# Performance work log

Hardware: AMD Instinct MI355X
Metric: run time of the kernel (lower is better)

## Reference

```python
import jax, jax.numpy as jnp
import numpy as np
import math

L = 12      # n_layer (alternating adaptive True/False)
H = 8       # n_head
C = 256     # n_embd
DH = C // H # head dim = 32
BS = 828    # block_size
T = 827     # seq len after dropping last token
VOCAB = 16384
CAM = 30
IMG = 256


def get_sinusoid(n_position, d_hid):
    pos = np.arange(n_position)[:, None].astype(np.float64)
    hid = np.arange(d_hid)[None, :]
    angle = pos / np.power(10000.0, 2.0 * (hid // 2) / d_hid)
    table = np.zeros_like(angle)
    table[:, 0::2] = np.sin(angle[:, 0::2])
    table[:, 1::2] = np.cos(angle[:, 1::2])
    return jnp.asarray(table[None], jnp.float32)  # [1, n_position, d_hid]


def layer_norm(x, w, b):
    m = x.mean(-1, keepdims=True)
    v = ((x - m) ** 2).mean(-1, keepdims=True)
    return (x - m) * jax.lax.rsqrt(v + 1e-5) * w + b


def setup_inputs() -> dict:
    key = jax.random.key(0)
    ks = iter(jax.random.split(key, 64))
    nrm = lambda shape, s=1.0: jax.random.normal(next(ks), shape, jnp.float32) * s
    B = 4
    inp = {
        'dc_emb': nrm((B, 572, C)),
        'z_emb': nrm((B, 256, C)),
        'p1': nrm((B, CAM)),
        'p2': nrm((B, CAM)),
        'p3': nrm((B, CAM)),
        'frame_emb': nrm((1, 256, C), 0.02),
        'camera_emb': nrm((1, 30, C), 0.02),
        'time_emb': get_sinusoid(BS, C),
        'loc_W1': nrm((2 * CAM, CAM), 0.02), 'loc_b1': jnp.zeros((2 * CAM,)),
        'loc_W2': nrm((IMG * IMG, 2 * CAM), 0.02), 'loc_b2': jnp.zeros((IMG * IMG,)),
        'ln1_w': jnp.ones((L, C)), 'ln1_b': jnp.zeros((L, C)),
        'Wq': nrm((L, C, C), 0.02), 'bq': jnp.zeros((L, C)),
        'Wk': nrm((L, C, C), 0.02), 'bk': jnp.zeros((L, C)),
        'Wv': nrm((L, C, C), 0.02), 'bv': jnp.zeros((L, C)),
        'Wo': nrm((L, C, C), 0.02), 'bo': jnp.zeros((L, C)),
        'ln2_w': jnp.ones((L, C)), 'ln2_b': jnp.zeros((L, C)),
        'W1': nrm((L, 4 * C, C), 0.02), 'b1': jnp.zeros((L, 4 * C)),
        'W2': nrm((L, C, 4 * C), 0.02), 'b2': jnp.zeros((L, C)),
        'lnf_w': jnp.ones((C,)), 'lnf_b': jnp.zeros((C,)),
        'head_W': nrm((VOCAB, C), 0.02),
    }
    return inp


def _forward(dc_emb, z_emb, p1, p2, p3, frame_emb, camera_emb, time_emb,
             loc_W1, loc_b1, loc_W2, loc_b2,
             ln1_w, ln1_b, Wq, bq, Wk, bk, Wv, bv, Wo, bo,
             ln2_w, ln2_b, W1, b1, W2, b2, lnf_w, lnf_b, head_W):
    B = dc_emb.shape[0]
    scale = 1.0 / math.sqrt(DH)

    # AdaptiveAttention bias h: [B, 1, BS, BS] with three 256x256 learned blocks
    def locality(p):
        z = jax.nn.gelu(p @ loc_W1.T + loc_b1, approximate=False)
        z = z @ loc_W2.T + loc_b2
        return z.reshape(B, IMG, IMG)

    h = jnp.zeros((B, 1, BS, BS), dc_emb.dtype)
    h = h.at[:, 0, 285:541, 0:256].set(locality(p1))
    h = h.at[:, 0, 571:827, 0:256].set(locality(p2))
    h = h.at[:, 0, 571:827, 286:542].set(locality(p3))
    h = h[:, :, :T, :T]

    # token + role + time embeddings
    tok = jnp.concatenate([dc_emb, z_emb], axis=1)[:, :-1, :]  # [B, T, C]
    role = jnp.concatenate([frame_emb, camera_emb, frame_emb, camera_emb, frame_emb], axis=1)[:, :T, :]
    x = tok + role + time_emb[:, :T, :]

    causal = jnp.tril(jnp.ones((T, T), bool))  # [T, T]

    for i in range(L):
        adaptive = (i % 2 == 0)
        xn = layer_norm(x, ln1_w[i], ln1_b[i])
        q = (xn @ Wq[i].T + bq[i]).reshape(B, T, H, DH)
        k = (xn @ Wk[i].T + bk[i]).reshape(B, T, H, DH)
        v = (xn @ Wv[i].T + bv[i]).reshape(B, T, H, DH)
        att = jnp.einsum('bqhd,bkhd->bhqk', q, k) * scale
        if adaptive:
            att = att + h
        att = jnp.where(causal, att, -jnp.inf)
        att = jax.nn.softmax(att, axis=-1)
        y = jnp.einsum('bhqk,bkhd->bqhd', att, v).reshape(B, T, C)
        x = x + y @ Wo[i].T + bo[i]
        xn2 = layer_norm(x, ln2_w[i], ln2_b[i])
        x = x + jax.nn.gelu(xn2 @ W1[i].T + b1[i], approximate=False) @ W2[i].T + b2[i]

    x = layer_norm(x, lnf_w, lnf_b)
    logits = x @ head_W.T  # [B, T, VOCAB]
    return logits


def reference(dc_emb, z_emb, p1, p2, p3, frame_emb, camera_emb, time_emb,
              loc_W1, loc_b1, loc_W2, loc_b2,
              ln1_w, ln1_b, Wq, bq, Wk, bk, Wv, bv, Wo, bo,
              ln2_w, ln2_b, W1, b1, W2, b2, lnf_w, lnf_b, head_W):
    return _forward(dc_emb, z_emb, p1, p2, p3, frame_emb, camera_emb, time_emb,
                    loc_W1, loc_b1, loc_W2, loc_b2,
                    ln1_w, ln1_b, Wq, bq, Wk, bk, Wv, bv, Wo, bo,
                    ln2_w, ln2_b, W1, b1, W2, b2, lnf_w, lnf_b, head_W)
```

## Files before the change

kernel.cpp:

```cpp
#include <hip/hip_runtime.h>
#include <hip/hip_bf16.h>
#include <math.h>

#define T_LEN 827
#define M_ROWS 3308
#define NLAYER 12
#define NEG_SENT -1e30f

typedef __attribute__((ext_vector_type(4))) float f32x4;
typedef __attribute__((ext_vector_type(8))) short bf16x8;

__device__ __forceinline__ float gelu_f(float x) {
    return 0.5f * x * (1.0f + erff(x * 0.70710678118654752440f));
}

__device__ __forceinline__ short f2bf_s(float x) {
    __hip_bfloat16 h = __float2bfloat16(x);
    return *reinterpret_cast<short*>(&h);
}

__global__ void cvt_kernel(const float* __restrict__ in, __hip_bfloat16* __restrict__ out, int n4) {
    int i = blockIdx.x * blockDim.x + threadIdx.x;
    if (i >= n4) return;
    float4 v = reinterpret_cast<const float4*>(in)[i];
    out[4*i+0] = __float2bfloat16(v.x);
    out[4*i+1] = __float2bfloat16(v.y);
    out[4*i+2] = __float2bfloat16(v.z);
    out[4*i+3] = __float2bfloat16(v.w);
}

__global__ void prep_wqkv_kernel(const float* __restrict__ Wq, const float* __restrict__ Wk,
                                 const float* __restrict__ Wv, __hip_bfloat16* __restrict__ out) {
    int i = blockIdx.x * 256 + threadIdx.x;
    if (i >= 12*768*64) return;
    int el = i * 4;
    int layer = el / (768*256);
    int rem = el % (768*256);
    int row = rem >> 8, col = rem & 255;
    const float* src;
    float sc = 1.f;
    if (row < 256)      { src = Wq + ((size_t)layer*256 + row)*256 + col; sc = 0.17677669529663687f; }
    else if (row < 512) { src = Wk + ((size_t)layer*256 + (row-256))*256 + col; }
    else                { src = Wv + ((size_t)layer*256 + (row-512))*256 + col; }
    float4 v = *reinterpret_cast<const float4*>(src);
    out[el+0] = __float2bfloat16(v.x * sc);
    out[el+1] = __float2bfloat16(v.y * sc);
    out[el+2] = __float2bfloat16(v.z * sc);
    out[el+3] = __float2bfloat16(v.w * sc);
}

__global__ void prep_bqkv_kernel(const float* __restrict__ bq, const float* __restrict__ bk,
                                 const float* __restrict__ bv, float* __restrict__ out) {
    int i = blockIdx.x * 256 + threadIdx.x;
    if (i >= 12*768) return;
    int layer = i / 768, row = i % 768;
    float v;
    if (row < 256)      v = bq[layer*256 + row] * 0.17677669529663687f;
    else if (row < 512) v = bk[layer*256 + (row-256)];
    else                v = bv[layer*256 + (row-512)];
    out[i] = v;
// ... 103 lines not shown
            *reinterpret_cast<uint4*>(&Bs[r][sg*8 + j*32]) =
                *reinterpret_cast<const uint4*>(bsrc + j*32);
    }
    int gr = m0 + r; if (gr > M-1) gr = M-1;
    {
        const __hip_bfloat16* asrc = Abf + (size_t)gr * 256 + sg * 8;
        #pragma unroll
        for (int j = 0; j < 8; ++j)
            *reinterpret_cast<uint4*>(&As[r][sg*8 + j*32]) =
                *reinterpret_cast<const uint4*>(asrc + j*32);
    }
    __syncthreads();

    const int wid = tid >> 6, lane = tid & 63;
    const int wm = wid >> 1, wn = wid & 1, c = lane & 15, g = lane >> 4;
    f32x4 acc[2][2];
    #pragma unroll
    for (int mi = 0; mi < 2; ++mi)
        #pragma unroll
        for (int ni = 0; ni < 2; ++ni)
            acc[mi][ni] = (f32x4){0.f, 0.f, 0.f, 0.f};

    #pragma unroll
    for (int kj = 0; kj < 8; ++kj) {
        bf16x8 a0 = *reinterpret_cast<const bf16x8*>(&As[wm*32 + c][kj*32 + g*8]);
        bf16x8 a1 = *reinterpret_cast<const bf16x8*>(&As[wm*32 + 16 + c][kj*32 + g*8]);
        bf16x8 b0 = *reinterpret_cast<const bf16x8*>(&Bs[wn*32 + c][kj*32 + g*8]);
        bf16x8 b1v = *reinterpret_cast<const bf16x8*>(&Bs[wn*32 + 16 + c][kj*32 + g*8]);
        acc[0][0] = __builtin_amdgcn_mfma_f32_16x16x32_bf16(a0, b0, acc[0][0], 0, 0, 0);
        acc[0][1] = __builtin_amdgcn_mfma_f32_16x16x32_bf16(a0, b1v, acc[0][1], 0, 0, 0);
        acc[1][0] = __builtin_amdgcn_mfma_f32_16x16x32_bf16(a1, b0, acc[1][0], 0, 0, 0);
        acc[1][1] = __builtin_amdgcn_mfma_f32_16x16x32_bf16(a1, b1v, acc[1][1], 0, 0, 0);
    }

    #pragma unroll
    for (int mi = 0; mi < 2; ++mi) {
        #pragma unroll
        for (int ni = 0; ni < 2; ++ni) {
            int n = n0 + wn*32 + ni*16 + c;
            float bb = bias ? bias[n] : 0.f;
            #pragma unroll
            for (int rg = 0; rg < 4; ++rg) {
                int m = m0 + wm*32 + mi*16 + g*4 + rg;
                if (m >= M) continue;
                float v = acc[mi][ni][rg] + bb;
                if (RESID) v += resid[(size_t)m*N + n];
                if (OUTBF16) ((__hip_bfloat16*)out)[(size_t)m*N + n] = __float2bfloat16(v);
                else         ((float*)out)[(size_t)m*N + n] = v;
            }
        }
    }
}

__global__ __launch_bounds__(512) void mlp_fused(
    float* __restrict__ x,
    const float* __restrict__ ln2w, const float* __restrict__ ln2b,
    const __hip_bfloat16* __restrict__ W1, const float* __restrict__ b1,
    const __hip_bfloat16* __restrict__ W2, const float* __restrict__ b2,
    const float* __restrict__ lnow, const float* __restrict__ lnob,
    __hip_bfloat16* __restrict__ xn)
{
    __shared__ __hip_bfloat16 As[32][264];
    __shared__ __hip_bfloat16 Ms[32][1044];
    const int tid = threadIdx.x;
    const int m0 = blockIdx.x * 32;
    const int w = tid >> 6, lane = tid & 63, c = lane & 15, g = lane >> 4;

    {
        int r = tid >> 4, p = tid & 15;
        int gr = m0 + r; if (gr > M_ROWS-1) gr = M_ROWS-1;
        const float* src = x + (size_t)gr*256 + p*16;
        float4 f0 = *reinterpret_cast<const float4*>(src);
        float4 f1 = *reinterpret_cast<const float4*>(src + 4);
        float4 f2 = *reinterpret_cast<const float4*>(src + 8);
        float4 f3 = *reinterpret_cast<const float4*>(src + 12);
        float vv[16] = {f0.x,f0.y,f0.z,f0.w, f1.x,f1.y,f1.z,f1.w,
                        f2.x,f2.y,f2.z,f2.w, f3.x,f3.y,f3.z,f3.w};
        float s = 0.f, q = 0.f;
        #pragma unroll
        for (int e = 0; e < 16; ++e) { s += vv[e]; q += vv[e]*vv[e]; }
        #pragma unroll
        for (int msk = 1; msk <= 8; msk <<= 1) { s += __shfl_xor(s, msk); q += __shfl_xor(q, msk); }
        float mean = s * (1.f/256.f);
        float rstd = rsqrtf(q*(1.f/256.f) - mean*mean + 1e-5f);
        bf16x8 pk0, pk1;
        #pragma unroll
        for (int e = 0; e < 8; ++e) {
            pk0[e] = f2bf_s((vv[e]   - mean)*rstd*ln2w[p*16+e]   + ln2b[p*16+e]);
            pk1[e] = f2bf_s((vv[8+e] - mean)*rstd*ln2w[p*16+8+e] + ln2b[p*16+8+e]);
        }
        *reinterpret_cast<bf16x8*>(&As[r][p*16])     = pk0;
        *reinterpret_cast<bf16x8*>(&As[r][p*16 + 8]) = pk1;
    }
    __syncthreads();

    #pragma unroll 1
    for (int ns = 0; ns < 8; ++ns) {
        int nb = w*128 + ns*16;
        const __hip_bfloat16* wrow = W1 + (size_t)(nb + c)*256 + g*8;
        f32x4 a0 = (f32x4){0.f,0.f,0.f,0.f}, a1 = (f32x4){0.f,0.f,0.f,0.f};
        #pragma unroll
        for (int kj = 0; kj < 8; ++kj) {
            bf16x8 bfrag = *reinterpret_cast<const bf16x8*>(wrow + kj*32);
            bf16x8 af0 = *reinterpret_cast<const bf16x8*>(&As[c][kj*32 + g*8]);
            bf16x8 af1 = *reinterpret_cast<const bf16x8*>(&As[16 + c][kj*32 + g*8]);
            a0 = __builtin_amdgcn_mfma_f32_16x16x32_bf16(af0, bfrag, a0, 0, 0, 0);
            a1 = __builtin_amdgcn_mfma_f32_16x16x32_bf16(af1, bfrag, a1, 0, 0, 0);
        }
        float bb = b1[nb + c];
        #pragma unroll
        for (int rg = 0; rg < 4; ++rg) {
            Ms[g*4 + rg][nb + c]      = __float2bfloat16(gelu_f(a0[rg] + bb));
            Ms[16 + g*4 + rg][nb + c] = __float2bfloat16(gelu_f(a1[rg] + bb));
        }
    }
    __syncthreads();

    f32x4 o[2][2];
    #pragma unroll
    for (int i = 0; i < 2; ++i)
        #pragma unroll
        for (int j = 0; j < 2; ++j)
            o[i][j] = (f32x4){0.f,0.f,0.f,0.f};
    #pragma unroll
    for (int ns2 = 0; ns2 < 2; ++ns2) {
        int nb = w*32 + ns2*16;
        const __hip_bfloat16* wrow = W2 + (size_t)(nb + c)*1024 + g*8;
        #pragma unroll
        for (int kj = 0; kj < 32; ++kj) {
            bf16x8 bfrag = *reinterpret_cast<const bf16x8*>(wrow + kj*32);
            bf16x8 af0 = *reinterpret_cast<const bf16x8*>(&Ms[c][kj*32 + g*8]);
            bf16x8 af1 = *reinterpret_cast<const bf16x8*>(&Ms[16 + c][kj*32 + g*8]);
            o[ns2][0] = __builtin_amdgcn_mfma_f32_16x16x32_bf16(af0, bfrag, o[ns2][0], 0, 0, 0);
            o[ns2][1] = __builtin_amdgcn_mfma_f32_16x16x32_bf16(af1, bfrag, o[ns2][1], 0, 0, 0);
        }
    }
    __syncthreads();

    float* xf = reinterpret_cast<float*>(&Ms[0][0]);
    #pragma unroll
    for (int ns2 = 0; ns2 < 2; ++ns2) {
        int nb = w*32 + ns2*16;
        float bb = b2[nb + c];
        #pragma unroll
        for (int mi = 0; mi < 2; ++mi) {
            #pragma unroll
            for (int rg = 0; rg < 4; ++rg) {
                int row = mi*16 + g*4 + rg;
                int gm = m0 + row;
                if (gm < M_ROWS) {
                    float v = o[ns2][mi][rg] + bb + x[(size_t)gm*256 + nb + c];
                    x[(size_t)gm*256 + nb + c] = v;
                    xf[row*256 + nb + c] = v;
                }
            }
        }
    }
    __syncthreads();

    {
        int r = tid >> 4, p = tid & 15;
        int gm = m0 + r;
        const float* src = xf + r*256 + p*16;
        float4 f0 = *reinterpret_cast<const float4*>(src);
        float4 f1 = *reinterpret_cast<const float4*>(src + 4);
        float4 f2 = *reinterpret_cast<const float4*>(src + 8);
        float4 f3 = *reinterpret_cast<const float4*>(src + 12);
        float vv[16] = {f0.x,f0.y,f0.z,f0.w, f1.x,f1.y,f1.z,f1.w,
                        f2.x,f2.y,f2.z,f2.w, f3.x,f3.y,f3.z,f3.w};
        float s = 0.f, q = 0.f;
        #pragma unroll
        for (int e = 0; e < 16; ++e) { s += vv[e]; q += vv[e]*vv[e]; }
        #pragma unroll
        for (int msk = 1; msk <= 8; msk <<= 1) { s += __shfl_xor(s, msk); q += __shfl_xor(q, msk); }
        float mean = s * (1.f/256.f);
        float rstd = rsqrtf(q*(1.f/256.f) - mean*mean + 1e-5f);
        if (gm < M_ROWS) {
            bf16x8 pk0, pk1;
            #pragma unroll
            for (int e = 0; e < 8; ++e) {
                pk0[e] = f2bf_s((vv[e]   - mean)*rstd*lnow[p*16+e]   + lnob[p*16+e]);
                pk1[e] = f2bf_s((vv[8+e] - mean)*rstd*lnow[p*16+8+e] + lnob[p*16+8+e]);
            }
            *reinterpret_cast<bf16x8*>(&xn[(size_t)gm*256 + p*16])     = pk0;
            *reinterpret_cast<bf16x8*>(&xn[(size_t)gm*256 + p*16 + 8]) = pk1;
        }
    }
}

template<int ADAPT>
__global__ __launch_bounds__(512) void attn_v3_kernel(const __hip_bfloat16* __restrict__ qkv,
                                                      const __hip_bfloat16* __restrict__ hbuf,
                                                      __hip_bfloat16* __restrict__ y) {
    const int qi = blockIdx.x, hh = blockIdx.y, b = blockIdx.z;
    const int tid = threadIdx.x;
    const int w = tid >> 6, lane = tid & 63;
    const int c = lane & 15, g = lane >> 4;
    const int qsub = w & 3, grp = w >> 2;
    const int q0 = qi * 64;
    const int qw0 = q0 + qsub * 16;
    const int nt = qi + 1;
    const int h = (nt + 1) >> 1;

    __shared__ short Ks[2][2][64][40];
    __shared__ short Vt[2][2][32][68];
    __shared__ short Pw[8][16][72];
    __shared__ float mlS[4][16][2];

    int qrow = qw0 + c; if (qrow > T_LEN-1) qrow = T_LEN-1;
    bf16x8 aq = *reinterpret_cast<const bf16x8*>(qkv + ((size_t)b*T_LEN + qrow)*768 + hh*32 + g*8);

    float m_r[4] = {NEG_SENT, NEG_SENT, NEG_SENT, NEG_SENT};
    float l_r[4] = {0.f, 0.f, 0.f, 0.f};
    f32x4 acc[2];
    acc[0] = (f32x4){0.f,0.f,0.f,0.f};
    acc[1] = (f32x4){0.f,0.f,0.f,0.f};

    const int lt = tid & 255;
    const int srow = lt >> 2;
    const int scol8 = (lt & 3) * 8;

    bf16x8 kreg, vreg;
    {
        int kb0 = (grp ? h : 0) * 64;
        int krow = kb0 + srow; if (krow > T_LEN-1) krow = T_LEN-1;
        const __hip_bfloat16* gb = qkv + ((size_t)b*T_LEN + krow)*768 + hh*32 + scol8;
        kreg = *reinterpret_cast<const bf16x8*>(gb + 256);
        vreg = *reinterpret_cast<const bf16x8*>(gb + 512);
    }

    for (int it = 0; it < h; ++it) {
        const int bsel = it & 1;
        const int kb = (grp ? h + it : it) * 64;
        *reinterpret_cast<bf16x8*>(&Ks[grp][bsel][srow][scol8]) = kreg;
        #pragma unroll
        for (int jj = 0; jj < 8; ++jj) Vt[grp][bsel][scol8 + jj][srow] = vreg[jj];
        __syncthreads();
        if (it + 1 < h) {
            int kbn = (grp ? h + it + 1 : it + 1) * 64;
            int krow = kbn + srow; if (krow > T_LEN-1) krow = T_LEN-1;
            const __hip_bfloat16* gb = qkv + ((size_t)b*T_LEN + krow)*768 + hh*32 + scol8;
            kreg = *reinterpret_cast<const bf16x8*>(gb + 256);
            vreg = *reinterpret_cast<const bf16x8*>(gb + 512);
        }

        f32x4 sc4[4];
        #pragma unroll
        for (int j = 0; j < 4; ++j) {
            bf16x8 bk = *reinterpret_cast<const bf16x8*>(&Ks[grp][bsel][j*16 + c][g*8]);
            sc4[j] = __builtin_amdgcn_mfma_f32_16x16x32_bf16(aq, bk, (f32x4){0.f,0.f,0.f,0.f}, 0, 0, 0);
        }

        float sv[4][4];
        #pragma unroll
        for (int j = 0; j < 4; ++j) {
            int kk = kb + j*16 + c;
            #pragma unroll
            for (int rg = 0; rg < 4; ++rg) {
                int qq = qw0 + g*4 + rg;
                bool valid = (qq < T_LEN) && (kk <= qq);
                float s = sc4[j][rg];
                if (ADAPT) s += valid ? __bfloat162float(hbuf[((size_t)b*T_LEN + qq)*T_LEN + kk]) : 0.f;
                sv[j][rg] = valid ? s : NEG_SENT;
            }
        }

        float sf[4];
        #pragma unroll
        for (int rg = 0; rg < 4; ++rg) {
            float m = fmaxf(fmaxf(sv[0][rg], sv[1][rg]), fmaxf(sv[2][rg], sv[3][rg]));
            #pragma unroll
            for (int msk = 1; msk <= 8; msk <<= 1) m = fmaxf(m, __shfl_xor(m, msk));
            float mn = fmaxf(m_r[rg], m);
            sf[rg] = __expf(m_r[rg] - mn);
            m_r[rg] = mn;
        }
        float p[4][4];
        #pragma unroll
        for (int rg = 0; rg < 4; ++rg) {
            float su = 0.f;
            #pragma unroll
            for (int j = 0; j < 4; ++j) {
                float e = __expf(sv[j][rg] - m_r[rg]);
                p[j][rg] = e;
                su += e;
            }
            #pragma unroll
            for (int msk = 1; msk <= 8; msk <<= 1) su += __shfl_xor(su, msk);
            l_r[rg] = l_r[rg] * sf[rg] + su;
            acc[0][rg] *= sf[rg];
            acc[1][rg] *= sf[rg];
        }

        #pragma unroll
        for (int j = 0; j < 4; ++j)
            #pragma unroll
            for (int rg = 0; rg < 4; ++rg)
                Pw[w][g*4 + rg][j*16 + c] = f2bf_s(p[j][rg]);

        #pragma unroll
        for (int kc = 0; kc < 2; ++kc) {
            bf16x8 ap = *reinterpret_cast<const bf16x8*>(&Pw[w][c][kc*32 + g*8]);
            #pragma unroll
            for (int dt = 0; dt < 2; ++dt) {
                bf16x8 bv = *reinterpret_cast<const bf16x8*>(&Vt[grp][bsel][dt*16 + c][kc*32 + g*8]);
                acc[dt] = __builtin_amdgcn_mfma_f32_16x16x32_bf16(ap, bv, acc[dt], 0, 0, 0);
            }
        }
    }

    if (grp == 1) {
        float* accS = reinterpret_cast<float*>(&Pw[4 + qsub][0][0]);
        #pragma unroll
        for (int rg = 0; rg < 4; ++rg) {
            int row = g*4 + rg;
            accS[row*32 + c]      = acc[0][rg];
            accS[row*32 + 16 + c] = acc[1][rg];
            if (c == 0) { mlS[qsub][row][0] = m_r[rg]; mlS[qsub][row][1] = l_r[rg]; }
        }
    }
    __syncthreads();
    if (grp == 0) {
        const float* accS = reinterpret_cast<const float*>(&Pw[4 + qsub][0][0]);
        #pragma unroll
        for (int rg = 0; rg < 4; ++rg) {
            int row = g*4 + rg;
            int qq = qw0 + row;
            if (qq >= T_LEN) continue;
            float m1 = mlS[qsub][row][0], l1 = mlS[qsub][row][1];
            float M = fmaxf(m_r[rg], m1);
            float a = __expf(m_r[rg] - M);
            float bsc = __expf(m1 - M);
            float L = l_r[rg]*a + l1*bsc;
            float inv = 1.f / L;
            float o0 = (acc[0][rg]*a + accS[row*32 + c]*bsc) * inv;
            float o1 = (acc[1][rg]*a + accS[row*32 + 16 + c]*bsc) * inv;
            size_t yo = ((size_t)b*T_LEN + qq)*256 + hh*32;
            y[yo + c]      = __float2bfloat16(o0);
            y[yo + 16 + c] = __float2bfloat16(o1);
        }
    }
}

extern "C" void kernel_launch(void* const* d_in, const int* in_sizes, int n_in,
                              void* d_out, int out_size, void* d_ws, size_t ws_size,
                              hipStream_t stream) {
    const float* dc    = (const float*)d_in[0];
    const float* zemb  = (const float*)d_in[1];
    const float* p1    = (const float*)d_in[2];
    const float* p2    = (const float*)d_in[3];
    const float* p3    = (const float*)d_in[4];
    const float* frame = (const float*)d_in[5];
    const float* cam   = (const float*)d_in[6];
    const float* timeE = (const float*)d_in[7];
    const float* locW1 = (const float*)d_in[8];
    const float* locb1 = (const float*)d_in[9];
    const float* locW2 = (const float*)d_in[10];
    const float* locb2 = (const float*)d_in[11];
    const float* ln1w  = (const float*)d_in[12];
    const float* ln1b  = (const float*)d_in[13];
    const float* Wq    = (const float*)d_in[14];
    const float* bq    = (const float*)d_in[15];
    const float* Wk    = (const float*)d_in[16];
    const float* bk    = (const float*)d_in[17];
    const float* Wv    = (const float*)d_in[18];
    const float* bv    = (const float*)d_in[19];
    const float* Wo    = (const float*)d_in[20];
    const float* bo    = (const float*)d_in[21];
    const float* ln2w  = (const float*)d_in[22];
    const float* ln2b  = (const float*)d_in[23];
    const float* W1p   = (const float*)d_in[24];
    const float* b1p   = (const float*)d_in[25];
    const float* W2p   = (const float*)d_in[26];
    const float* b2p   = (const float*)d_in[27];
    const float* lnfw  = (const float*)d_in[28];
    const float* lnfb  = (const float*)d_in[29];
    const float* headW = (const float*)d_in[30];

    char* wsb = (char*)d_ws;
    size_t off = 0;
    auto alloc = [&](size_t bytes) -> char* {
        char* p = wsb + off;
        off += (bytes + 255) & ~(size_t)255;
        return p;
    };
    __hip_bfloat16* wqkv_bf = (__hip_bfloat16*)alloc(12ull*768*256*2);
    float*          bqkv    = (float*)alloc(12ull*768*4);
    __hip_bfloat16* wo_bf = (__hip_bfloat16*)alloc(12ull*65536*2);
    __hip_bfloat16* w1_bf = (__hip_bfloat16*)alloc(12ull*262144*2);
    __hip_bfloat16* w2_bf = (__hip_bfloat16*)alloc(12ull*262144*2);
    __hip_bfloat16* wh_bf = (__hip_bfloat16*)alloc(16384ull*256*2);
    __hip_bfloat16* hbuf = (__hip_bfloat16*)alloc(4ull*T_LEN*T_LEN*2);
    float* x    = (float*)alloc((size_t)M_ROWS*256*4);
    __hip_bfloat16* xn   = (__hip_bfloat16*)alloc((size_t)M_ROWS*256*2);
    __hip_bfloat16* qkvb = (__hip_bfloat16*)alloc((size_t)M_ROWS*768*2);
    __hip_bfloat16* yb   = (__hip_bfloat16*)alloc((size_t)M_ROWS*256*2);
    float* z1   = (float*)alloc(720*4);

    prep_wqkv_kernel<<<(12*768*64 + 255)/256, 256, 0, stream>>>(Wq, Wk, Wv, wqkv_bf);
    prep_bqkv_kernel<<<36, 256, 0, stream>>>(bq, bk, bv, bqkv);
    cvt_kernel<<<768, 256, 0, stream>>>(Wo, wo_bf, 196608);
    cvt_kernel<<<3072, 256, 0, stream>>>(W1p, w1_bf, 786432);
    cvt_kernel<<<3072, 256, 0, stream>>>(W2p, w2_bf, 786432);
    cvt_kernel<<<4096, 256, 0, stream>>>(headW, wh_bf, 1048576);

    loc_z1_kernel<<<1, 256, 0, stream>>>(p1, p2, p3, locW1, locb1, z1);
    zero_kernel<<<2048, 256, 0, stream>>>((float*)hbuf, (4*T_LEN*T_LEN)/2);
    h_fill_kernel<<<256, 256, 0, stream>>>(z1, locW2, locb2, hbuf);

    init_x_kernel<<<M_ROWS, 256, 0, stream>>>(dc, zemb, frame, cam, timeE, x);
    ln_kernel<<<M_ROWS, 256, 0, stream>>>(x, ln1w, ln1b, xn);

    dim3 gqkv(52, 12);
    dim3 goproj(52, 4);
    dim3 gattn(13, 8, 4);

    for (int i = 0; i < NLAYER; ++i) {
        gemm_k256<false,true><<<gqkv, 256, 0, stream>>>(
            xn, wqkv_bf + (size_t)i*196608, bqkv + i*768, nullptr, qkvb, M_ROWS, 768);
        if (i % 2 == 0) attn_v3_kernel<1><<<gattn, 512, 0, stream>>>(qkvb, hbuf, yb);
        else            attn_v3_kernel<0><<<gattn, 512, 0, stream>>>(qkvb, hbuf, yb);
        gemm_k256<true,false><<<goproj, 256, 0, stream>>>(
            yb, wo_bf + (size_t)i*65536, bo + i*256, x, x, M_ROWS, 256);
        const float* lnow = (i == NLAYER-1) ? lnfw : (ln1w + (i+1)*256);
        const float* lnob = (i == NLAYER-1) ? lnfb : (ln1b + (i+1)*256);
        mlp_fused<<<104, 512, 0, stream>>>(
            x, ln2w + i*256, ln2b + i*256,
            w1_bf + (size_t)i*262144, b1p + i*1024,
            w2_bf + (size_t)i*262144, b2p + i*256, lnow, lnob, xn);
    }

    gemm_k256<false,false><<<dim3(52, 256), 256, 0, stream>>>(
        xn, wh_bf, nullptr, nullptr, (float*)d_out, M_ROWS, 16384);
}
```

Before: 1.249 ms.

## Emit transposed V from QKV GEMM and stream K/V from global in attention

The QKV projection becomes a dedicated kernel that writes Q/K into a 512-wide buffer and V pre-transposed per batch and head into a padded buffer. Attention now gives each wavefront its own 16-query tile, reading K and V^T straight from global memory into registers with register prefetch. This removes LDS staging, block-wide barriers and the split-KV merge step. In exchange each wave reloads K/V from global or L2 with no sharing across waves, the block shrinks to 256 threads, and the V writes in the GEMM epilogue are scattered.

```diff
diff --git a/kernel.cpp b/kernel.cpp
--- a/kernel.cpp
+++ b/kernel.cpp
@@ -6,6 +6,7 @@
 #define M_ROWS 3308
 #define NLAYER 12
 #define NEG_SENT -1e30f
+#define VT_W 896
 
 typedef __attribute__((ext_vector_type(4))) float f32x4;
 typedef __attribute__((ext_vector_type(8))) short bf16x8;
@@ -215,6 +216,83 @@
     }
 }
 
+__global__ __launch_bounds__(256) void gemm_qkv256(
+    const __hip_bfloat16* __restrict__ Abf,
+    const __hip_bfloat16* __restrict__ W, const float* __restrict__ bias,
+    __hip_bfloat16* __restrict__ qkout, __hip_bfloat16* __restrict__ vTout)
+{
+    __shared__ __hip_bfloat16 As[64][264];
+    __shared__ __hip_bfloat16 Bs[64][264];
+    const int tid = threadIdx.x;
+    const int m0 = blockIdx.x * 64, n0 = blockIdx.y * 64;
+    const int r = tid >> 2, sg = tid & 3;
+
+    {
+        const __hip_bfloat16* bsrc = W + (size_t)(n0 + r) * 256 + sg * 8;
+        #pragma unroll
+        for (int j = 0; j < 8; ++j)
+            *reinterpret_cast<uint4*>(&Bs[r][sg*8 + j*32]) =
+                *reinterpret_cast<const uint4*>(bsrc + j*32);
+    }
+    int gr = m0 + r; if (gr > M_ROWS-1) gr = M_ROWS-1;
+    {
+        const __hip_bfloat16* asrc = Abf + (size_t)gr * 256 + sg * 8;
+        #pragma unroll
+        for (int j = 0; j < 8; ++j)
+            *reinterpret_cast<uint4*>(&As[r][sg*8 + j*32]) =
+                *reinterpret_cast<const uint4*>(asrc + j*32);
+    }
+    __syncthreads();
+
+    const int wid = tid >> 6, lane = tid & 63;
+    const int wm = wid >> 1, wn = wid & 1, c = lane & 15, g = lane >> 4;
+    f32x4 acc[2][2];
+    #pragma unroll
+    for (int mi = 0; mi < 2; ++mi)
+        #pragma unroll
+        for (int ni = 0; ni < 2; ++ni)
+            acc[mi][ni] = (f32x4){0.f, 0.f, 0.f, 0.f};
+
+    #pragma unroll
+    for (int kj = 0; kj < 8; ++kj) {
+        bf16x8 a0 = *reinterpret_cast<const bf16x8*>(&As[wm*32 + c][kj*32 + g*8]);
+        bf16x8 a1 = *reinterpret_cast<const bf16x8*>(&As[wm*32 + 16 + c][kj*32 + g*8]);
+        bf16x8 b0 = *reinterpret_cast<const bf16x8*>(&Bs[wn*32 + c][kj*32 + g*8]);
+        bf16x8 b1v = *reinterpret_cast<const bf16x8*>(&Bs[wn*32 + 16 + c][kj*32 + g*8]);
+        acc[0][0] = __builtin_amdgcn_mfma_f32_16x16x32_bf16(a0, b0, acc[0][0], 0, 0, 0);
+        acc[0][1] = __builtin_amdgcn_mfma_f32_16x16x32_bf16(a0, b1v, acc[0][1], 0, 0, 0);
+        acc[1][0] = __builtin_amdgcn_mfma_f32_16x16x32_bf16(a1, b0, acc[1][0], 0, 0, 0);
+        acc[1][1] = __builtin_amdgcn_mfma_f32_16x16x32_bf16(a1, b1v, acc[1][1], 0, 0, 0);
+    }
+
+    #pragma unroll
+    for (int mi = 0; mi < 2; ++mi) {
+        #pragma unroll
+        for (int ni = 0; ni < 2; ++ni) {
+            int n = n0 + wn*32 + ni*16 + c;
+            float bb = bias[n];
+            if (n < 512) {
+                #pragma unroll
+                for (int rg = 0; rg < 4; ++rg) {
+                    int m = m0 + wm*32 + mi*16 + g*4 + rg;
+                    if (m >= M_ROWS) continue;
+                    qkout[(size_t)m*512 + n] = __float2bfloat16(acc[mi][ni][rg] + bb);
+                }
+            } else {
+                int rel = n - 512, hh = rel >> 5, dh = rel & 31;
+                #pragma unroll
+                for (int rg = 0; rg < 4; ++rg) {
+                    int m = m0 + wm*32 + mi*16 + g*4 + rg;
+                    if (m >= M_ROWS) continue;
+                    int bq = m / T_LEN, t = m - bq*T_LEN;
+                    vTout[((size_t)((bq*8 + hh)*32) + dh)*VT_W + t] =
+                        __float2bfloat16(acc[mi][ni][rg] + bb);
+                }
+            }
+        }
+    }
+}
+
 __global__ __launch_bounds__(512) void mlp_fused(
     float* __restrict__ x,
     const float* __restrict__ ln2w, const float* __restrict__ ln2b,
@@ -352,26 +430,26 @@
 }
 
 template<int ADAPT>
-__global__ __launch_bounds__(512) void attn_v3_kernel(const __hip_bfloat16* __restrict__ qkv,
+__global__ __launch_bounds__(256) void attn_v4_kernel(const __hip_bfloat16* __restrict__ qk,
+                                                      const __hip_bfloat16* __restrict__ vT,
                                                       const __hip_bfloat16* __restrict__ hbuf,
                                                       __hip_bfloat16* __restrict__ y) {
-    const int qi = blockIdx.x, hh = blockIdx.y, b = blockIdx.z;
+    const int hh = blockIdx.y, b = blockIdx.z;
     const int tid = threadIdx.x;
     const int w = tid >> 6, lane = tid & 63;
     const int c = lane & 15, g = lane >> 4;
-    const int qsub = w & 3, grp = w >> 2;
-    const int q0 = qi * 64;
-    const int qw0 = q0 + qsub * 16;
-    const int nt = qi + 1;
-    const int h = (nt + 1) >> 1;
-
-    __shared__ short Ks[2][2][64][40];
-    __shared__ short Vt[2][2][32][68];
-    __shared__ short Pw[8][16][72];
-    __shared__ float mlS[4][16][2];
-
-    int qrow = qw0 + c; if (qrow > T_LEN-1) qrow = T_LEN-1;
-    bf16x8 aq = *reinterpret_cast<const bf16x8*>(qkv + ((size_t)b*T_LEN + qrow)*768 + hh*32 + g*8);
+    const int jt = blockIdx.x * 4 + w;
+    const int q0 = jt * 16;
+    const int nit = (q0 + 15) / 64 + 1;
+
+    __shared__ short Pw[4][16][72];
+
+    const size_t qkb = (size_t)b * T_LEN * 512;
+    int qrow = q0 + c; if (qrow > T_LEN-1) qrow = T_LEN-1;
+    bf16x8 aq = *reinterpret_cast<const bf16x8*>(qk + qkb + (size_t)qrow*512 + hh*32 + g*8);
+
+    const __hip_bfloat16* kbase = qk + qkb + 256 + hh*32 + g*8;
+    const __hip_bfloat16* vbase = vT + (size_t)((b*8 + hh)*32)*VT_W + g*8;
 
     float m_r[4] = {NEG_SENT, NEG_SENT, NEG_SENT, NEG_SENT};
     float l_r[4] = {0.f, 0.f, 0.f, 0.f};
@@ -379,52 +457,52 @@
     acc[0] = (f32x4){0.f,0.f,0.f,0.f};
     acc[1] = (f32x4){0.f,0.f,0.f,0.f};
 
-    const int lt = tid & 255;
-    const int srow = lt >> 2;
-    const int scol8 = (lt & 3) * 8;
-
-    bf16x8 kreg, vreg;
-    {
-        int kb0 = (grp ? h : 0) * 64;
-        int krow = kb0 + srow; if (krow > T_LEN-1) krow = T_LEN-1;
-        const __hip_bfloat16* gb = qkv + ((size_t)b*T_LEN + krow)*768 + hh*32 + scol8;
-        kreg = *reinterpret_cast<const bf16x8*>(gb + 256);
-        vreg = *reinterpret_cast<const bf16x8*>(gb + 512);
-    }
-
-    for (int it = 0; it < h; ++it) {
-        const int bsel = it & 1;
-        const int kb = (grp ? h + it : it) * 64;
-        *reinterpret_cast<bf16x8*>(&Ks[grp][bsel][srow][scol8]) = kreg;
-        #pragma unroll
-        for (int jj = 0; jj < 8; ++jj) Vt[grp][bsel][scol8 + jj][srow] = vreg[jj];
-        __syncthreads();
-        if (it + 1 < h) {
-            int kbn = (grp ? h + it + 1 : it + 1) * 64;
-            int krow = kbn + srow; if (krow > T_LEN-1) krow = T_LEN-1;
-            const __hip_bfloat16* gb = qkv + ((size_t)b*T_LEN + krow)*768 + hh*32 + scol8;
-            kreg = *reinterpret_cast<const bf16x8*>(gb + 256);
-            vreg = *reinterpret_cast<const bf16x8*>(gb + 512);
-        }
+    bf16x8 bk[4], bv[2][2];
+    #pragma unroll
+    for (int jj = 0; jj < 4; ++jj) {
+        int krow = jj*16 + c; if (krow > T_LEN-1) krow = T_LEN-1;
+        bk[jj] = *reinterpret_cast<const bf16x8*>(kbase + (size_t)krow*512);
+    }
+    #pragma unroll
+    for (int dt = 0; dt < 2; ++dt)
+        #pragma unroll
+        for (int kc = 0; kc < 2; ++kc)
+            bv[dt][kc] = *reinterpret_cast<const bf16x8*>(vbase + (size_t)(dt*16 + c)*VT_W + kc*32);
+
+    for (int it = 0; it < nit; ++it) {
+        const int kb = it * 64;
 
         f32x4 sc4[4];
         #pragma unroll
-        for (int j = 0; j < 4; ++j) {
-            bf16x8 bk = *reinterpret_cast<const bf16x8*>(&Ks[grp][bsel][j*16 + c][g*8]);
-            sc4[j] = __builtin_amdgcn_mfma_f32_16x16x32_bf16(aq, bk, (f32x4){0.f,0.f,0.f,0.f}, 0, 0, 0);
+        for (int jj = 0; jj < 4; ++jj)
+            sc4[jj] = __builtin_amdgcn_mfma_f32_16x16x32_bf16(aq, bk[jj], (f32x4){0.f,0.f,0.f,0.f}, 0, 0, 0);
+
+        bf16x8 nk[4], nv[2][2];
+        if (it + 1 < nit) {
+            const int kbn = kb + 64;
+            #pragma unroll
+            for (int jj = 0; jj < 4; ++jj) {
+                int krow = kbn + jj*16 + c; if (krow > T_LEN-1) krow = T_LEN-1;
+                nk[jj] = *reinterpret_cast<const bf16x8*>(kbase + (size_t)krow*512);
+            }
+            #pragma unroll
+            for (int dt = 0; dt < 2; ++dt)
+                #pragma unroll
+                for (int kc = 0; kc < 2; ++kc)
+                    nv[dt][kc] = *reinterpret_cast<const bf16x8*>(vbase + (size_t)(dt*16 + c)*VT_W + kbn + kc*32);
         }
 
         float sv[4][4];
         #pragma unroll
-        for (int j = 0; j < 4; ++j) {
-            int kk = kb + j*16 + c;
+        for (int jj = 0; jj < 4; ++jj) {
+            int kk = kb + jj*16 + c;
             #pragma unroll
             for (int rg = 0; rg < 4; ++rg) {
-                int qq = qw0 + g*4 + rg;
+                int qq = q0 + g*4 + rg;
                 bool valid = (qq < T_LEN) && (kk <= qq);
-                float s = sc4[j][rg];
+                float s = sc4[jj][rg];
                 if (ADAPT) s += valid ? __bfloat162float(hbuf[((size_t)b*T_LEN + qq)*T_LEN + kk]) : 0.f;
-                sv[j][rg] = valid ? s : NEG_SENT;
+                sv[jj][rg] = valid ? s : NEG_SENT;
             }
         }
 
@@ -443,9 +521,9 @@
         for (int rg = 0; rg < 4; ++rg) {
             float su = 0.f;
             #pragma unroll
-            for (int j = 0; j < 4; ++j) {
-                float e = __expf(sv[j][rg] - m_r[rg]);
-                p[j][rg] = e;
+            for (int jj = 0; jj < 4; ++jj) {
+                float e = __expf(sv[jj][rg] - m_r[rg]);
+                p[jj][rg] = e;
                 su += e;
             }
             #pragma unroll
@@ -456,52 +534,37 @@
         }
 
         #pragma unroll
-        for (int j = 0; j < 4; ++j)
+        for (int jj = 0; jj < 4; ++jj)
             #pragma unroll
             for (int rg = 0; rg < 4; ++rg)
-                Pw[w][g*4 + rg][j*16 + c] = f2bf_s(p[j][rg]);
+                Pw[w][g*4 + rg][jj*16 + c] = f2bf_s(p[jj][rg]);
 
         #pragma unroll
         for (int kc = 0; kc < 2; ++kc) {
             bf16x8 ap = *reinterpret_cast<const bf16x8*>(&Pw[w][c][kc*32 + g*8]);
             #pragma unroll
-            for (int dt = 0; dt < 2; ++dt) {
-                bf16x8 bv = *reinterpret_cast<const bf16x8*>(&Vt[grp][bsel][dt*16 + c][kc*32 + g*8]);
-                acc[dt] = __builtin_amdgcn_mfma_f32_16x16x32_bf16(ap, bv, acc[dt], 0, 0, 0);
-            }
-        }
-    }
-
-    if (grp == 1) {
-        float* accS = reinterpret_cast<float*>(&Pw[4 + qsub][0][0]);
-        #pragma unroll
-        for (int rg = 0; rg < 4; ++rg) {
-            int row = g*4 + rg;
-            accS[row*32 + c]      = acc[0][rg];
-            accS[row*32 + 16 + c] = acc[1][rg];
-            if (c == 0) { mlS[qsub][row][0] = m_r[rg]; mlS[qsub][row][1] = l_r[rg]; }
-        }
-    }
-    __syncthreads();
-    if (grp == 0) {
-        const float* accS = reinterpret_cast<const float*>(&Pw[4 + qsub][0][0]);
-        #pragma unroll
-        for (int rg = 0; rg < 4; ++rg) {
-            int row = g*4 + rg;
-            int qq = qw0 + row;
-            if (qq >= T_LEN) continue;
-            float m1 = mlS[qsub][row][0], l1 = mlS[qsub][row][1];
-            float M = fmaxf(m_r[rg], m1);
-            float a = __expf(m_r[rg] - M);
-            float bsc = __expf(m1 - M);
-            float L = l_r[rg]*a + l1*bsc;
-            float inv = 1.f / L;
-            float o0 = (acc[0][rg]*a + accS[row*32 + c]*bsc) * inv;
-            float o1 = (acc[1][rg]*a + accS[row*32 + 16 + c]*bsc) * inv;
-            size_t yo = ((size_t)b*T_LEN + qq)*256 + hh*32;
-            y[yo + c]      = __float2bfloat16(o0);
-            y[yo + 16 + c] = __float2bfloat16(o1);
-        }
+            for (int dt = 0; dt < 2; ++dt)
+                acc[dt] = __builtin_amdgcn_mfma_f32_16x16x32_bf16(ap, bv[dt][kc], acc[dt], 0, 0, 0);
+        }
+
+        if (it + 1 < nit) {
+            #pragma unroll
+            for (int jj = 0; jj < 4; ++jj) bk[jj] = nk[jj];
+            #pragma unroll
+            for (int dt = 0; dt < 2; ++dt)
+                #pragma unroll
+                for (int kc = 0; kc < 2; ++kc) bv[dt][kc] = nv[dt][kc];
+        }
+    }
+
+    #pragma unroll
+    for (int rg = 0; rg < 4; ++rg) {
+        int qq = q0 + g*4 + rg;
+        if (qq >= T_LEN) continue;
+        float inv = 1.f / l_r[rg];
+        size_t yo = ((size_t)b*T_LEN + qq)*256 + hh*32;
+        y[yo + c]      = __float2bfloat16(acc[0][rg] * inv);
+        y[yo + 16 + c] = __float2bfloat16(acc[1][rg] * inv);
     }
 }
 
@@ -556,7 +619,8 @@
     __hip_bfloat16* hbuf = (__hip_bfloat16*)alloc(4ull*T_LEN*T_LEN*2);
     float* x    = (float*)alloc((size_t)M_ROWS*256*4);
     __hip_bfloat16* xn   = (__hip_bfloat16*)alloc((size_t)M_ROWS*256*2);
-    __hip_bfloat16* qkvb = (__hip_bfloat16*)alloc((size_t)M_ROWS*768*2);
+    __hip_bfloat16* qkb  = (__hip_bfloat16*)alloc((size_t)M_ROWS*512*2);
+    __hip_bfloat16* vTb  = (__hip_bfloat16*)alloc(1024ull*VT_W*2);
     __hip_bfloat16* yb   = (__hip_bfloat16*)alloc((size_t)M_ROWS*256*2);
     float* z1   = (float*)alloc(720*4);
 
@@ -579,10 +643,10 @@
     dim3 gattn(13, 8, 4);
 
     for (int i = 0; i < NLAYER; ++i) {
-        gemm_k256<false,true><<<gqkv, 256, 0, stream>>>(
-            xn, wqkv_bf + (size_t)i*196608, bqkv + i*768, nullptr, qkvb, M_ROWS, 768);
-        if (i % 2 == 0) attn_v3_kernel<1><<<gattn, 512, 0, stream>>>(qkvb, hbuf, yb);
-        else            attn_v3_kernel<0><<<gattn, 512, 0, stream>>>(qkvb, hbuf, yb);
+        gemm_qkv256<<<gqkv, 256, 0, stream>>>(
+            xn, wqkv_bf + (size_t)i*196608, bqkv + i*768, qkb, vTb);
+        if (i % 2 == 0) attn_v4_kernel<1><<<gattn, 256, 0, stream>>>(qkb, vTb, hbuf, yb);
+        else            attn_v4_kernel<0><<<gattn, 256, 0, stream>>>(qkb, vTb, hbuf, yb);
         gemm_k256<true,false><<<goproj, 256, 0, stream>>>(
             yb, wo_bf + (size_t)i*65536, bo + i*256, x, x, M_ROWS, 256);
         const float* lnow = (i == NLAYER-1) ? lnfw : (ln1w + (i+1)*256);
```

New measurement: 1.483 ms. 1.19x slower.

## Halve MLP row tile and replace split-K attention with single-group 128-key tiles

Applied to the files above, without the earlier changes.

The fused MLP kernel now processes 16 rows per block instead of 32, doubling the grid to 207 blocks so more CUs are busy, at the cost of reading each weight matrix twice as often. The attention kernel drops its two-group key split with cross-group softmax merge and register double buffering. It now uses 256 threads, each block walking key tiles of 128 with a single flash-style online softmax. This removes the merge step and the shared-memory reduction, but loses load prefetch overlap and serialises the key loop per block.

```diff
diff --git a/kernel.cpp b/kernel.cpp
--- a/kernel.cpp
+++ b/kernel.cpp
@@ -223,37 +223,31 @@
     const float* __restrict__ lnow, const float* __restrict__ lnob,
     __hip_bfloat16* __restrict__ xn)
 {
-    __shared__ __hip_bfloat16 As[32][264];
-    __shared__ __hip_bfloat16 Ms[32][1044];
+    __shared__ __hip_bfloat16 As[16][264];
+    __shared__ __hip_bfloat16 Ms[16][1044];
     const int tid = threadIdx.x;
-    const int m0 = blockIdx.x * 32;
+    const int m0 = blockIdx.x * 16;
     const int w = tid >> 6, lane = tid & 63, c = lane & 15, g = lane >> 4;
 
     {
-        int r = tid >> 4, p = tid & 15;
+        int r = tid >> 5, p = tid & 31;
         int gr = m0 + r; if (gr > M_ROWS-1) gr = M_ROWS-1;
-        const float* src = x + (size_t)gr*256 + p*16;
+        const float* src = x + (size_t)gr*256 + p*8;
         float4 f0 = *reinterpret_cast<const float4*>(src);
         float4 f1 = *reinterpret_cast<const float4*>(src + 4);
-        float4 f2 = *reinterpret_cast<const float4*>(src + 8);
-        float4 f3 = *reinterpret_cast<const float4*>(src + 12);
-        float vv[16] = {f0.x,f0.y,f0.z,f0.w, f1.x,f1.y,f1.z,f1.w,
-                        f2.x,f2.y,f2.z,f2.w, f3.x,f3.y,f3.z,f3.w};
+        float vv[8] = {f0.x,f0.y,f0.z,f0.w, f1.x,f1.y,f1.z,f1.w};
         float s = 0.f, q = 0.f;
         #pragma unroll
-        for (int e = 0; e < 16; ++e) { s += vv[e]; q += vv[e]*vv[e]; }
-        #pragma unroll
-        for (int msk = 1; msk <= 8; msk <<= 1) { s += __shfl_xor(s, msk); q += __shfl_xor(q, msk); }
+        for (int e = 0; e < 8; ++e) { s += vv[e]; q += vv[e]*vv[e]; }
+        #pragma unroll
+        for (int msk = 1; msk <= 16; msk <<= 1) { s += __shfl_xor(s, msk); q += __shfl_xor(q, msk); }
         float mean = s * (1.f/256.f);
         float rstd = rsqrtf(q*(1.f/256.f) - mean*mean + 1e-5f);
-        bf16x8 pk0, pk1;
-        #pragma unroll
-        for (int e = 0; e < 8; ++e) {
-            pk0[e] = f2bf_s((vv[e]   - mean)*rstd*ln2w[p*16+e]   + ln2b[p*16+e]);
-            pk1[e] = f2bf_s((vv[8+e] - mean)*rstd*ln2w[p*16+8+e] + ln2b[p*16+8+e]);
-        }
-        *reinterpret_cast<bf16x8*>(&As[r][p*16])     = pk0;
-        *reinterpret_cast<bf16x8*>(&As[r][p*16 + 8]) = pk1;
+        bf16x8 pk;
+        #pragma unroll
+        for (int e = 0; e < 8; ++e)
+            pk[e] = f2bf_s((vv[e] - mean)*rstd*ln2w[p*8+e] + ln2b[p*8+e]);
+        *reinterpret_cast<bf16x8*>(&As[r][p*8]) = pk;
     }
     __syncthreads();
 
@@ -261,30 +255,23 @@
     for (int ns = 0; ns < 8; ++ns) {
         int nb = w*128 + ns*16;
         const __hip_bfloat16* wrow = W1 + (size_t)(nb + c)*256 + g*8;
-        f32x4 a0 = (f32x4){0.f,0.f,0.f,0.f}, a1 = (f32x4){0.f,0.f,0.f,0.f};
+        f32x4 a0 = (f32x4){0.f,0.f,0.f,0.f};
         #pragma unroll
         for (int kj = 0; kj < 8; ++kj) {
             bf16x8 bfrag = *reinterpret_cast<const bf16x8*>(wrow + kj*32);
             bf16x8 af0 = *reinterpret_cast<const bf16x8*>(&As[c][kj*32 + g*8]);
-            bf16x8 af1 = *reinterpret_cast<const bf16x8*>(&As[16 + c][kj*32 + g*8]);
             a0 = __builtin_amdgcn_mfma_f32_16x16x32_bf16(af0, bfrag, a0, 0, 0, 0);
-            a1 = __builtin_amdgcn_mfma_f32_16x16x32_bf16(af1, bfrag, a1, 0, 0, 0);
         }
         float bb = b1[nb + c];
         #pragma unroll
-        for (int rg = 0; rg < 4; ++rg) {
-            Ms[g*4 + rg][nb + c]      = __float2bfloat16(gelu_f(a0[rg] + bb));
-            Ms[16 + g*4 + rg][nb + c] = __float2bfloat16(gelu_f(a1[rg] + bb));
-        }
-    }
-    __syncthreads();
-
-    f32x4 o[2][2];
-    #pragma unroll
-    for (int i = 0; i < 2; ++i)
-        #pragma unroll
-        for (int j = 0; j < 2; ++j)
-            o[i][j] = (f32x4){0.f,0.f,0.f,0.f};
+        for (int rg = 0; rg < 4; ++rg)
+            Ms[g*4 + rg][nb + c] = __float2bfloat16(gelu_f(a0[rg] + bb));
+    }
+    __syncthreads();
+
+    f32x4 o[2];
+    o[0] = (f32x4){0.f,0.f,0.f,0.f};
+    o[1] = (f32x4){0.f,0.f,0.f,0.f};
     #pragma unroll
     for (int ns2 = 0; ns2 < 2; ++ns2) {
         int nb = w*32 + ns2*16;
@@ -293,9 +280,7 @@
         for (int kj = 0; kj < 32; ++kj) {
             bf16x8 bfrag = *reinterpret_cast<const bf16x8*>(wrow + kj*32);
             bf16x8 af0 = *reinterpret_cast<const bf16x8*>(&Ms[c][kj*32 + g*8]);
-            bf16x8 af1 = *reinterpret_cast<const bf16x8*>(&Ms[16 + c][kj*32 + g*8]);
-            o[ns2][0] = __builtin_amdgcn_mfma_f32_16x16x32_bf16(af0, bfrag, o[ns2][0], 0, 0, 0);
-            o[ns2][1] = __builtin_amdgcn_mfma_f32_16x16x32_bf16(af1, bfrag, o[ns2][1], 0, 0, 0);
+            o[ns2] = __builtin_amdgcn_mfma_f32_16x16x32_bf16(af0, bfrag, o[ns2], 0, 0, 0);
         }
     }
     __syncthreads();
@@ -306,69 +291,56 @@
         int nb = w*32 + ns2*16;
         float bb = b2[nb + c];
         #pragma unroll
-        for (int mi = 0; mi < 2; ++mi) {
-            #pragma unroll
-            for (int rg = 0; rg < 4; ++rg) {
-                int row = mi*16 + g*4 + rg;
-                int gm = m0 + row;
-                if (gm < M_ROWS) {
-                    float v = o[ns2][mi][rg] + bb + x[(size_t)gm*256 + nb + c];
-                    x[(size_t)gm*256 + nb + c] = v;
-                    xf[row*256 + nb + c] = v;
-                }
+        for (int rg = 0; rg < 4; ++rg) {
+            int row = g*4 + rg;
+            int gm = m0 + row;
+            if (gm < M_ROWS) {
+                float v = o[ns2][rg] + bb + x[(size_t)gm*256 + nb + c];
+                x[(size_t)gm*256 + nb + c] = v;
+                xf[row*256 + nb + c] = v;
             }
         }
     }
     __syncthreads();
 
     {
-        int r = tid >> 4, p = tid & 15;
+        int r = tid >> 5, p = tid & 31;
         int gm = m0 + r;
-        const float* src = xf + r*256 + p*16;
+        const float* src = xf + r*256 + p*8;
         float4 f0 = *reinterpret_cast<const float4*>(src);
         float4 f1 = *reinterpret_cast<const float4*>(src + 4);
-        float4 f2 = *reinterpret_cast<const float4*>(src + 8);
-        float4 f3 = *reinterpret_cast<const float4*>(src + 12);
-        float vv[16] = {f0.x,f0.y,f0.z,f0.w, f1.x,f1.y,f1.z,f1.w,
-                        f2.x,f2.y,f2.z,f2.w, f3.x,f3.y,f3.z,f3.w};
+        float vv[8] = {f0.x,f0.y,f0.z,f0.w, f1.x,f1.y,f1.z,f1.w};
         float s = 0.f, q = 0.f;
         #pragma unroll
-        for (int e = 0; e < 16; ++e) { s += vv[e]; q += vv[e]*vv[e]; }
-        #pragma unroll
-        for (int msk = 1; msk <= 8; msk <<= 1) { s += __shfl_xor(s, msk); q += __shfl_xor(q, msk); }
+        for (int e = 0; e < 8; ++e) { s += vv[e]; q += vv[e]*vv[e]; }
+        #pragma unroll
+        for (int msk = 1; msk <= 16; msk <<= 1) { s += __shfl_xor(s, msk); q += __shfl_xor(q, msk); }
         float mean = s * (1.f/256.f);
         float rstd = rsqrtf(q*(1.f/256.f) - mean*mean + 1e-5f);
         if (gm < M_ROWS) {
-            bf16x8 pk0, pk1;
-            #pragma unroll
-            for (int e = 0; e < 8; ++e) {
-                pk0[e] = f2bf_s((vv[e]   - mean)*rstd*lnow[p*16+e]   + lnob[p*16+e]);
-                pk1[e] = f2bf_s((vv[8+e] - mean)*rstd*lnow[p*16+8+e] + lnob[p*16+8+e]);
-            }
-            *reinterpret_cast<bf16x8*>(&xn[(size_t)gm*256 + p*16])     = pk0;
-            *reinterpret_cast<bf16x8*>(&xn[(size_t)gm*256 + p*16 + 8]) = pk1;
+            bf16x8 pk;
+            #pragma unroll
+            for (int e = 0; e < 8; ++e)
+                pk[e] = f2bf_s((vv[e] - mean)*rstd*lnow[p*8+e] + lnob[p*8+e]);
+            *reinterpret_cast<bf16x8*>(&xn[(size_t)gm*256 + p*8]) = pk;
         }
     }
 }
 
 template<int ADAPT>
-__global__ __launch_bounds__(512) void attn_v3_kernel(const __hip_bfloat16* __restrict__ qkv,
-                                                      const __hip_bfloat16* __restrict__ hbuf,
-                                                      __hip_bfloat16* __restrict__ y) {
+__global__ __launch_bounds__(256) void attn_mfma_kernel(const __hip_bfloat16* __restrict__ qkv,
+                                                        const __hip_bfloat16* __restrict__ hbuf,
+                                                        __hip_bfloat16* __restrict__ y) {
     const int qi = blockIdx.x, hh = blockIdx.y, b = blockIdx.z;
     const int tid = threadIdx.x;
     const int w = tid >> 6, lane = tid & 63;
     const int c = lane & 15, g = lane >> 4;
-    const int qsub = w & 3, grp = w >> 2;
     const int q0 = qi * 64;
-    const int qw0 = q0 + qsub * 16;
-    const int nt = qi + 1;
-    const int h = (nt + 1) >> 1;
-
-    __shared__ short Ks[2][2][64][40];
-    __shared__ short Vt[2][2][32][68];
-    __shared__ short Pw[8][16][72];
-    __shared__ float mlS[4][16][2];
+    const int qw0 = q0 + w * 16;
+
+    __shared__ short Ks[128][40];
+    __shared__ short Vt[32][136];
+    __shared__ short Pw[4][16][136];
 
     int qrow = qw0 + c; if (qrow > T_LEN-1) qrow = T_LEN-1;
     bf16x8 aq = *reinterpret_cast<const bf16x8*>(qkv + ((size_t)b*T_LEN + qrow)*768 + hh*32 + g*8);
@@ -379,50 +351,47 @@
     acc[0] = (f32x4){0.f,0.f,0.f,0.f};
     acc[1] = (f32x4){0.f,0.f,0.f,0.f};
 
-    const int lt = tid & 255;
-    const int srow = lt >> 2;
-    const int scol8 = (lt & 3) * 8;
-
-    bf16x8 kreg, vreg;
-    {
-        int kb0 = (grp ? h : 0) * 64;
-        int krow = kb0 + srow; if (krow > T_LEN-1) krow = T_LEN-1;
-        const __hip_bfloat16* gb = qkv + ((size_t)b*T_LEN + krow)*768 + hh*32 + scol8;
-        kreg = *reinterpret_cast<const bf16x8*>(gb + 256);
-        vreg = *reinterpret_cast<const bf16x8*>(gb + 512);
-    }
-
-    for (int it = 0; it < h; ++it) {
-        const int bsel = it & 1;
-        const int kb = (grp ? h + it : it) * 64;
-        *reinterpret_cast<bf16x8*>(&Ks[grp][bsel][srow][scol8]) = kreg;
-        #pragma unroll
-        for (int jj = 0; jj < 8; ++jj) Vt[grp][bsel][scol8 + jj][srow] = vreg[jj];
+    const int nk = min(q0 + 64, T_LEN);
+    const int nit = (nk + 127) >> 7;
+    const int srow = tid >> 1;
+    const int half = tid & 1;
+
+    for (int it = 0; it < nit; ++it) {
+        const int kb = it * 128;
+        {
+            int krow = kb + srow; if (krow > T_LEN-1) krow = T_LEN-1;
+            const __hip_bfloat16* gb = qkv + ((size_t)b*T_LEN + krow)*768 + hh*32 + half*16;
+            uint4 k0 = *reinterpret_cast<const uint4*>(gb + 256);
+            uint4 k1 = *reinterpret_cast<const uint4*>(gb + 256 + 8);
+            *reinterpret_cast<uint4*>(&Ks[srow][half*16])     = k0;
+            *reinterpret_cast<uint4*>(&Ks[srow][half*16 + 8]) = k1;
+            bf16x8 v0 = *reinterpret_cast<const bf16x8*>(gb + 512);
+            bf16x8 v1 = *reinterpret_cast<const bf16x8*>(gb + 512 + 8);
+            #pragma unroll
+            for (int jj = 0; jj < 8; ++jj) {
+                Vt[half*16 + jj][srow]     = v0[jj];
+                Vt[half*16 + 8 + jj][srow] = v1[jj];
+            }
+        }
         __syncthreads();
-        if (it + 1 < h) {
-            int kbn = (grp ? h + it + 1 : it + 1) * 64;
-            int krow = kbn + srow; if (krow > T_LEN-1) krow = T_LEN-1;
-            const __hip_bfloat16* gb = qkv + ((size_t)b*T_LEN + krow)*768 + hh*32 + scol8;
-            kreg = *reinterpret_cast<const bf16x8*>(gb + 256);
-            vreg = *reinterpret_cast<const bf16x8*>(gb + 512);
-        }
-
-        f32x4 sc4[4];
-        #pragma unroll
-        for (int j = 0; j < 4; ++j) {
-            bf16x8 bk = *reinterpret_cast<const bf16x8*>(&Ks[grp][bsel][j*16 + c][g*8]);
-            sc4[j] = __builtin_amdgcn_mfma_f32_16x16x32_bf16(aq, bk, (f32x4){0.f,0.f,0.f,0.f}, 0, 0, 0);
-        }
-
-        float sv[4][4];
-        #pragma unroll
-        for (int j = 0; j < 4; ++j) {
+
+        float sv[8][4];
+        #pragma unroll
+        for (int j = 0; j < 8; ++j) {
+            bf16x8 bk = *reinterpret_cast<const bf16x8*>(&Ks[j*16 + c][g*8]);
+            f32x4 s4 = __builtin_amdgcn_mfma_f32_16x16x32_bf16(aq, bk, (f32x4){0.f,0.f,0.f,0.f}, 0, 0, 0);
+            #pragma unroll
+            for (int rg = 0; rg < 4; ++rg) sv[j][rg] = s4[rg];
+        }
+
+        #pragma unroll
+        for (int j = 0; j < 8; ++j) {
             int kk = kb + j*16 + c;
             #pragma unroll
             for (int rg = 0; rg < 4; ++rg) {
                 int qq = qw0 + g*4 + rg;
                 bool valid = (qq < T_LEN) && (kk <= qq);
-                float s = sc4[j][rg];
+                float s = sv[j][rg];
                 if (ADAPT) s += valid ? __bfloat162float(hbuf[((size_t)b*T_LEN + qq)*T_LEN + kk]) : 0.f;
                 sv[j][rg] = valid ? s : NEG_SENT;
             }
@@ -431,21 +400,22 @@
         float sf[4];
         #pragma unroll
         for (int rg = 0; rg < 4; ++rg) {
-            float m = fmaxf(fmaxf(sv[0][rg], sv[1][rg]), fmaxf(sv[2][rg], sv[3][rg]));
+            float m = sv[0][rg];
+            #pragma unroll
+            for (int j = 1; j < 8; ++j) m = fmaxf(m, sv[j][rg]);
             #pragma unroll
             for (int msk = 1; msk <= 8; msk <<= 1) m = fmaxf(m, __shfl_xor(m, msk));
             float mn = fmaxf(m_r[rg], m);
             sf[rg] = __expf(m_r[rg] - mn);
             m_r[rg] = mn;
         }
-        float p[4][4];
         #pragma unroll
         for (int rg = 0; rg < 4; ++rg) {
             float su = 0.f;
             #pragma unroll
-            for (int j = 0; j < 4; ++j) {
+            for (int j = 0; j < 8; ++j) {
                 float e = __expf(sv[j][rg] - m_r[rg]);
-                p[j][rg] = e;
+                sv[j][rg] = e;
                 su += e;
             }
             #pragma unroll
@@ -456,52 +426,31 @@
         }
 
         #pragma unroll
-        for (int j = 0; j < 4; ++j)
+        for (int j = 0; j < 8; ++j)
             #pragma unroll
             for (int rg = 0; rg < 4; ++rg)
-                Pw[w][g*4 + rg][j*16 + c] = f2bf_s(p[j][rg]);
-
-        #pragma unroll
-        for (int kc = 0; kc < 2; ++kc) {
+                Pw[w][g*4 + rg][j*16 + c] = f2bf_s(sv[j][rg]);
+
+        #pragma unroll
+        for (int kc = 0; kc < 4; ++kc) {
             bf16x8 ap = *reinterpret_cast<const bf16x8*>(&Pw[w][c][kc*32 + g*8]);
             #pragma unroll
             for (int dt = 0; dt < 2; ++dt) {
-                bf16x8 bv = *reinterpret_cast<const bf16x8*>(&Vt[grp][bsel][dt*16 + c][kc*32 + g*8]);
+                bf16x8 bv = *reinterpret_cast<const bf16x8*>(&Vt[dt*16 + c][kc*32 + g*8]);
                 acc[dt] = __builtin_amdgcn_mfma_f32_16x16x32_bf16(ap, bv, acc[dt], 0, 0, 0);
             }
         }
-    }
-
-    if (grp == 1) {
-        float* accS = reinterpret_cast<float*>(&Pw[4 + qsub][0][0]);
-        #pragma unroll
-        for (int rg = 0; rg < 4; ++rg) {
-            int row = g*4 + rg;
-            accS[row*32 + c]      = acc[0][rg];
-            accS[row*32 + 16 + c] = acc[1][rg];
-            if (c == 0) { mlS[qsub][row][0] = m_r[rg]; mlS[qsub][row][1] = l_r[rg]; }
-        }
-    }
-    __syncthreads();
-    if (grp == 0) {
-        const float* accS = reinterpret_cast<const float*>(&Pw[4 + qsub][0][0]);
-        #pragma unroll
-        for (int rg = 0; rg < 4; ++rg) {
-            int row = g*4 + rg;
-            int qq = qw0 + row;
-            if (qq >= T_LEN) continue;
-            float m1 = mlS[qsub][row][0], l1 = mlS[qsub][row][1];
-            float M = fmaxf(m_r[rg], m1);
-            float a = __expf(m_r[rg] - M);
-            float bsc = __expf(m1 - M);
-            float L = l_r[rg]*a + l1*bsc;
-            float inv = 1.f / L;
-            float o0 = (acc[0][rg]*a + accS[row*32 + c]*bsc) * inv;
-            float o1 = (acc[1][rg]*a + accS[row*32 + 16 + c]*bsc) * inv;
-            size_t yo = ((size_t)b*T_LEN + qq)*256 + hh*32;
-            y[yo + c]      = __float2bfloat16(o0);
-            y[yo + 16 + c] = __float2bfloat16(o1);
-        }
+        __syncthreads();
+    }
+
+    #pragma unroll
+    for (int rg = 0; rg < 4; ++rg) {
+        int qq = qw0 + g*4 + rg;
+        if (qq >= T_LEN) continue;
+        float inv = 1.f / l_r[rg];
+        size_t yo = ((size_t)b*T_LEN + qq)*256 + hh*32;
+        y[yo + c]      = __float2bfloat16(acc[0][rg] * inv);
+        y[yo + 16 + c] = __float2bfloat16(acc[1][rg] * inv);
     }
 }
 
@@ -581,13 +530,13 @@
     for (int i = 0; i < NLAYER; ++i) {
         gemm_k256<false,true><<<gqkv, 256, 0, stream>>>(
             xn, wqkv_bf + (size_t)i*196608, bqkv + i*768, nullptr, qkvb, M_ROWS, 768);
-        if (i % 2 == 0) attn_v3_kernel<1><<<gattn, 512, 0, stream>>>(qkvb, hbuf, yb);
-        else            attn_v3_kernel<0><<<gattn, 512, 0, stream>>>(qkvb, hbuf, yb);
+        if (i % 2 == 0) attn_mfma_kernel<1><<<gattn, 256, 0, stream>>>(qkvb, hbuf, yb);
+        else            attn_mfma_kernel<0><<<gattn, 256, 0, stream>>>(qkvb, hbuf, yb);
         gemm_k256<true,false><<<goproj, 256, 0, stream>>>(
             yb, wo_bf + (size_t)i*65536, bo + i*256, x, x, M_ROWS, 256);
         const float* lnow = (i == NLAYER-1) ? lnfw : (ln1w + (i+1)*256);
         const float* lnob = (i == NLAYER-1) ? lnfb : (ln1b + (i+1)*256);
-        mlp_fused<<<104, 512, 0, stream>>>(
+        mlp_fused<<<207, 512, 0, stream>>>(
             x, ln2w + i*256, ln2b + i*256,
             w1_bf + (size_t)i*262144, b1p + i*1024,
             w2_bf + (size_t)i*262144, b2p + i*256, lnow, lnob, xn);
```

New measurement: 1.414 ms. 1.13x slower.
